# Performance work log

Hardware: AMD Instinct MI355X
Metric: run time of the kernel (lower is better)

## Reference

```python
import jax, jax.numpy as jnp
import numpy as np

D = 8388608  # vector_dim
N = 1024     # phase table size
M = 1024     # magnitude table size


def setup_inputs() -> dict:
    key = jax.random.key(0)
    k1, k2, k3, k4 = jax.random.split(key, 4)
    ctx_phase_idx = jax.random.randint(k1, (D,), 0, N, dtype=jnp.int64)
    ctx_mag_idx = jax.random.randint(k2, (D,), 0, M, dtype=jnp.int64)
    self_phase_idx = jax.random.randint(k3, (D,), 0, N, dtype=jnp.int64)
    self_mag_idx = jax.random.randint(k4, (D,), 0, M, dtype=jnp.int64)
    # Lookup tables (the ExtendedLookupTableModule's precomputed tables):
    # phase table = cos(2*pi*i/N), its grad = -sin(2*pi*i/N) * (2*pi/N)
    # magnitude table = exp(linspace), its grad = same exp * slope
    phase_grid = 2.0 * jnp.pi * jnp.arange(N, dtype=jnp.float32) / N
    mag_grid = jnp.linspace(-1.0, 1.0, M, dtype=jnp.float32)
    cos_table = jnp.cos(phase_grid)
    cos_grad_table = -jnp.sin(phase_grid) * (2.0 * jnp.pi / N)
    exp_table = jnp.exp(mag_grid)
    exp_grad_table = exp_table * (2.0 / (M - 1))
    return {
        "ctx_phase_idx": ctx_phase_idx,
        "ctx_mag_idx": ctx_mag_idx,
        "self_phase_idx": self_phase_idx,
        "self_mag_idx": self_mag_idx,
        "cos_table": cos_table,
        "exp_table": exp_table,
        "cos_grad_table": cos_grad_table,
        "exp_grad_table": exp_grad_table,
    }


def reference(ctx_phase_idx, ctx_mag_idx, self_phase_idx, self_mag_idx,
              cos_table, exp_table, cos_grad_table, exp_grad_table):
    # mod-indexed sums
    phase_out = (ctx_phase_idx + self_phase_idx) % N  # [D] int
    mag_out = (ctx_mag_idx + self_mag_idx) % M        # [D] int
    # four table gathers
    cos_vals = cos_table[phase_out]       # [D]
    exp_vals = exp_table[mag_out]         # [D]
    dcos = cos_grad_table[phase_out]      # [D]
    dexp = exp_grad_table[mag_out]        # [D]
    # elementwise multiplies + reduction
    signal = cos_vals * exp_vals          # [D]
    grad_phase = dcos * exp_vals          # [D]
    grad_mag = cos_vals * dexp            # [D]
    strength = signal.sum()
    return (phase_out, mag_out, signal, strength, grad_phase, grad_mag)
```

## Files before the change

kernel.cpp:

```cpp
#include <hip/hip_runtime.h>

constexpr int D_TOTAL = 8388608;
constexpr int TBL = 1024;
constexpr int IDX_MASK = 1023;
constexpr int BLOCK = 256;
constexpr int VEC = 4;
constexpr int ELEMS_PER_BLOCK = BLOCK * VEC;
constexpr int NBLOCKS = D_TOTAL / ELEMS_PER_BLOCK;

__global__ __launch_bounds__(BLOCK) void phasecell_main(
    const int* __restrict__ ctx_p, const int* __restrict__ ctx_m,
    const int* __restrict__ self_p, const int* __restrict__ self_m,
    const float* __restrict__ cos_t, const float* __restrict__ exp_t,
    const float* __restrict__ dcos_t, const float* __restrict__ dexp_t,
    float* __restrict__ out, float* __restrict__ block_sums) {
  __shared__ float2 s_phase[TBL];
  __shared__ float2 s_mag[TBL];
  for (int i = threadIdx.x; i < TBL; i += BLOCK) {
    s_phase[i] = make_float2(cos_t[i], dcos_t[i]);
    s_mag[i]   = make_float2(exp_t[i], dexp_t[i]);
  }
  __syncthreads();

  const int base = (blockIdx.x * BLOCK + threadIdx.x) * VEC;

  const int4 cp = *reinterpret_cast<const int4*>(ctx_p + base);
  const int4 cm = *reinterpret_cast<const int4*>(ctx_m + base);
  const int4 sp = *reinterpret_cast<const int4*>(self_p + base);
  const int4 sm = *reinterpret_cast<const int4*>(self_m + base);

  int p[VEC], m[VEC];
  p[0] = (cp.x + sp.x) & IDX_MASK;  m[0] = (cm.x + sm.x) & IDX_MASK;
  p[1] = (cp.y + sp.y) & IDX_MASK;  m[1] = (cm.y + sm.y) & IDX_MASK;
  p[2] = (cp.z + sp.z) & IDX_MASK;  m[2] = (cm.z + sm.z) & IDX_MASK;
  p[3] = (cp.w + sp.w) & IDX_MASK;  m[3] = (cm.w + sm.w) & IDX_MASK;

  float4 po, mo, sig;
  float gph[VEC], gmg[VEC];
  float local = 0.f;
#pragma unroll
  for (int j = 0; j < VEC; ++j) {
    const float2 ph = s_phase[p[j]];
    const float2 mg = s_mag[m[j]];
    const float s = ph.x * mg.x;
    (&sig.x)[j] = s;
    gph[j] = ph.y * mg.x;
    gmg[j] = ph.x * mg.y;
    (&po.x)[j] = (float)p[j];
    (&mo.x)[j] = (float)m[j];
    local += s;
  }

  *reinterpret_cast<float4*>(out + base)              = po;
  *reinterpret_cast<float4*>(out + D_TOTAL + base)    = mo;
  *reinterpret_cast<float4*>(out + 2 * D_TOTAL + base) = sig;

  float* gp_base = out + 3 * D_TOTAL + 1 + base;
  float* gm_base = out + 4 * D_TOTAL + 1 + base;
#pragma unroll
  for (int j = 0; j < VEC; ++j) {
    gp_base[j] = gph[j];
    gm_base[j] = gmg[j];
  }

#pragma unroll
  for (int off = 32; off > 0; off >>= 1) local += __shfl_down(local, off, 64);
  __shared__ float wsum[BLOCK / 64];
  const int wave = threadIdx.x >> 6;
  const int lane = threadIdx.x & 63;
  if (lane == 0) wsum[wave] = local;
  __syncthreads();
  if (threadIdx.x == 0) {
    float t = 0.f;
#pragma unroll
    for (int w = 0; w < BLOCK / 64; ++w) t += wsum[w];
    block_sums[blockIdx.x] = t;
  }
}

__global__ __launch_bounds__(BLOCK) void phasecell_reduce(
    const float* __restrict__ partials, float* __restrict__ strength_out) {
  float s = 0.f;
  for (int i = threadIdx.x; i < NBLOCKS; i += BLOCK) s += partials[i];
#pragma unroll
  for (int off = 32; off > 0; off >>= 1) s += __shfl_down(s, off, 64);
  __shared__ float wsum[BLOCK / 64];
  const int wave = threadIdx.x >> 6;
  const int lane = threadIdx.x & 63;
  if (lane == 0) wsum[wave] = s;
  __syncthreads();
  if (threadIdx.x == 0) {
    float t = 0.f;
#pragma unroll
    for (int w = 0; w < BLOCK / 64; ++w) t += wsum[w];
    strength_out[0] = t;
  }
}

extern "C" void kernel_launch(void* const* d_in, const int* in_sizes, int n_in,
                              void* d_out, int out_size, void* d_ws, size_t ws_size,
                              hipStream_t stream) {
  const int* ctx_p  = (const int*)d_in[0];
  const int* ctx_m  = (const int*)d_in[1];
  const int* self_p = (const int*)d_in[2];
  const int* self_m = (const int*)d_in[3];
  const float* cos_t  = (const float*)d_in[4];
  const float* exp_t  = (const float*)d_in[5];
  const float* dcos_t = (const float*)d_in[6];
  const float* dexp_t = (const float*)d_in[7];
  float* out = (float*)d_out;
  float* block_sums = (float*)d_ws;

  phasecell_main<<<NBLOCKS, BLOCK, 0, stream>>>(
      ctx_p, ctx_m, self_p, self_m, cos_t, exp_t, dcos_t, dexp_t, out, block_sums);
  phasecell_reduce<<<1, BLOCK, 0, stream>>>(block_sums, out + 3 * (size_t)D_TOTAL);
}
```

Before: 294.4 us.

## Fuse final reduction via last-block atomic counter and use nontemporal loads/stores

Merges the separate single-block reduction kernel into the main kernel: each block publishes its partial sum, bumps an atomic counter, and the last block to finish sums all partials and writes the strength. A memset resets the counter before each launch. All streaming input loads and output stores are also switched to nontemporal builtins to avoid polluting caches on this purely streaming workload. This removes one kernel launch and its tail latency but adds a memset launch and an atomic plus fence per block.

```diff
diff --git a/kernel.cpp b/kernel.cpp
--- a/kernel.cpp
+++ b/kernel.cpp
@@ -8,12 +8,16 @@
 constexpr int ELEMS_PER_BLOCK = BLOCK * VEC;
 constexpr int NBLOCKS = D_TOTAL / ELEMS_PER_BLOCK;
 
-__global__ __launch_bounds__(BLOCK) void phasecell_main(
+typedef float f32x4 __attribute__((ext_vector_type(4)));
+typedef int   i32x4 __attribute__((ext_vector_type(4)));
+
+__global__ __launch_bounds__(BLOCK) void phasecell_fused(
     const int* __restrict__ ctx_p, const int* __restrict__ ctx_m,
     const int* __restrict__ self_p, const int* __restrict__ self_m,
     const float* __restrict__ cos_t, const float* __restrict__ exp_t,
     const float* __restrict__ dcos_t, const float* __restrict__ dexp_t,
-    float* __restrict__ out, float* __restrict__ block_sums) {
+    float* __restrict__ out, float* __restrict__ partials,
+    unsigned int* __restrict__ counter) {
   __shared__ float2 s_phase[TBL];
   __shared__ float2 s_mag[TBL];
   for (int i = threadIdx.x; i < TBL; i += BLOCK) {
@@ -24,18 +28,19 @@
 
   const int base = (blockIdx.x * BLOCK + threadIdx.x) * VEC;
 
-  const int4 cp = *reinterpret_cast<const int4*>(ctx_p + base);
-  const int4 cm = *reinterpret_cast<const int4*>(ctx_m + base);
-  const int4 sp = *reinterpret_cast<const int4*>(self_p + base);
-  const int4 sm = *reinterpret_cast<const int4*>(self_m + base);
+  const i32x4 cp = __builtin_nontemporal_load((const i32x4*)(ctx_p + base));
+  const i32x4 cm = __builtin_nontemporal_load((const i32x4*)(ctx_m + base));
+  const i32x4 sp = __builtin_nontemporal_load((const i32x4*)(self_p + base));
+  const i32x4 sm = __builtin_nontemporal_load((const i32x4*)(self_m + base));
 
   int p[VEC], m[VEC];
-  p[0] = (cp.x + sp.x) & IDX_MASK;  m[0] = (cm.x + sm.x) & IDX_MASK;
-  p[1] = (cp.y + sp.y) & IDX_MASK;  m[1] = (cm.y + sm.y) & IDX_MASK;
-  p[2] = (cp.z + sp.z) & IDX_MASK;  m[2] = (cm.z + sm.z) & IDX_MASK;
-  p[3] = (cp.w + sp.w) & IDX_MASK;  m[3] = (cm.w + sm.w) & IDX_MASK;
+#pragma unroll
+  for (int j = 0; j < VEC; ++j) {
+    p[j] = (cp[j] + sp[j]) & IDX_MASK;
+    m[j] = (cm[j] + sm[j]) & IDX_MASK;
+  }
 
-  float4 po, mo, sig;
+  f32x4 po, mo, sig;
   float gph[VEC], gmg[VEC];
   float local = 0.f;
 #pragma unroll
@@ -43,24 +48,24 @@
     const float2 ph = s_phase[p[j]];
     const float2 mg = s_mag[m[j]];
     const float s = ph.x * mg.x;
-    (&sig.x)[j] = s;
+    sig[j] = s;
     gph[j] = ph.y * mg.x;
     gmg[j] = ph.x * mg.y;
-    (&po.x)[j] = (float)p[j];
-    (&mo.x)[j] = (float)m[j];
+    po[j] = (float)p[j];
+    mo[j] = (float)m[j];
     local += s;
   }
 
-  *reinterpret_cast<float4*>(out + base)              = po;
-  *reinterpret_cast<float4*>(out + D_TOTAL + base)    = mo;
-  *reinterpret_cast<float4*>(out + 2 * D_TOTAL + base) = sig;
+  __builtin_nontemporal_store(po,  (f32x4*)(out + base));
+  __builtin_nontemporal_store(mo,  (f32x4*)(out + D_TOTAL + base));
+  __builtin_nontemporal_store(sig, (f32x4*)(out + 2 * D_TOTAL + base));
 
   float* gp_base = out + 3 * D_TOTAL + 1 + base;
   float* gm_base = out + 4 * D_TOTAL + 1 + base;
 #pragma unroll
   for (int j = 0; j < VEC; ++j) {
-    gp_base[j] = gph[j];
-    gm_base[j] = gmg[j];
+    __builtin_nontemporal_store(gph[j], gp_base + j);
+    __builtin_nontemporal_store(gmg[j], gm_base + j);
   }
 
 #pragma unroll
@@ -74,26 +79,30 @@
     float t = 0.f;
 #pragma unroll
     for (int w = 0; w < BLOCK / 64; ++w) t += wsum[w];
-    block_sums[blockIdx.x] = t;
+    partials[blockIdx.x] = t;
   }
-}
 
-__global__ __launch_bounds__(BLOCK) void phasecell_reduce(
-    const float* __restrict__ partials, float* __restrict__ strength_out) {
-  float s = 0.f;
-  for (int i = threadIdx.x; i < NBLOCKS; i += BLOCK) s += partials[i];
+  __shared__ bool s_last;
+  if (threadIdx.x == 0) {
+    __threadfence();
+    unsigned int prev = atomicAdd(counter, 1u);
+    s_last = (prev == NBLOCKS - 1);
+  }
+  __syncthreads();
+  if (s_last) {
+    __threadfence();
+    float s = 0.f;
+    for (int i = threadIdx.x; i < NBLOCKS; i += BLOCK) s += partials[i];
 #pragma unroll
-  for (int off = 32; off > 0; off >>= 1) s += __shfl_down(s, off, 64);
-  __shared__ float wsum[BLOCK / 64];
-  const int wave = threadIdx.x >> 6;
-  const int lane = threadIdx.x & 63;
-  if (lane == 0) wsum[wave] = s;
-  __syncthreads();
-  if (threadIdx.x == 0) {
-    float t = 0.f;
+    for (int off = 32; off > 0; off >>= 1) s += __shfl_down(s, off, 64);
+    if (lane == 0) wsum[wave] = s;
+    __syncthreads();
+    if (threadIdx.x == 0) {
+      float t = 0.f;
 #pragma unroll
-    for (int w = 0; w < BLOCK / 64; ++w) t += wsum[w];
-    strength_out[0] = t;
+      for (int w = 0; w < BLOCK / 64; ++w) t += wsum[w];
+      out[3 * (size_t)D_TOTAL] = t;
+    }
   }
 }
 
@@ -109,9 +118,12 @@
   const float* dcos_t = (const float*)d_in[6];
   const float* dexp_t = (const float*)d_in[7];
   float* out = (float*)d_out;
-  float* block_sums = (float*)d_ws;
+  float* partials = (float*)d_ws;
+  unsigned int* counter = (unsigned int*)((char*)d_ws + NBLOCKS * sizeof(float));
 
-  phasecell_main<<<NBLOCKS, BLOCK, 0, stream>>>(
-      ctx_p, ctx_m, self_p, self_m, cos_t, exp_t, dcos_t, dexp_t, out, block_sums);
-  phasecell_reduce<<<1, BLOCK, 0, stream>>>(block_sums, out + 3 * (size_t)D_TOTAL);
+  hipMemsetAsync(counter, 0, sizeof(unsigned int), stream);
+
+  phasecell_fused<<<NBLOCKS, BLOCK, 0, stream>>>(
+      ctx_p, ctx_m, self_p, self_m, cos_t, exp_t, dcos_t, dexp_t,
+      out, partials, counter);
 }
```

Measured after the change: 666.3 us. 2.26x slower.
